# Kernel tuning notes

Hardware: AMD Instinct MI355X
Metric: run time of the kernel (lower is better)

## Reference

```python
import jax, jax.numpy as jnp
import numpy as np

N_NODES = 100000
N_EDGES = 1600000
D_IN, D_HID, D_OUT = 128, 128, 64


def setup_inputs() -> dict:
    key = jax.random.key(0)
    ks = jax.random.split(key, 6)
    x = jax.random.normal(ks[0], (N_NODES, D_IN), dtype=jnp.float32)
    edge_index = jax.random.randint(ks[1], (2, N_EDGES), 0, N_NODES, dtype=jnp.int64)
    s1 = 1.0 / np.sqrt(D_IN)
    s2 = 1.0 / np.sqrt(D_HID)
    return {
        "x": x,
        "edge_index": edge_index,
        "Wl1": jax.random.uniform(ks[2], (D_HID, D_IN), jnp.float32, -s1, s1),
        "bl1": jnp.zeros((D_HID,), jnp.float32),
        "Wr1": jax.random.uniform(ks[3], (D_HID, D_IN), jnp.float32, -s1, s1),
        "Wl2": jax.random.uniform(ks[4], (D_OUT, D_HID), jnp.float32, -s2, s2),
        "bl2": jnp.zeros((D_OUT,), jnp.float32),
        "Wr2": jax.random.uniform(ks[5], (D_OUT, D_HID), jnp.float32, -s2, s2),
    }


def _sage_conv(x, src, dst, Wl, bl, Wr, n_nodes):
    # mean-aggregate neighbor features src -> dst
    agg = jax.ops.segment_sum(x[src], dst, num_segments=n_nodes)  # [N, d_in]
    deg = jax.ops.segment_sum(jnp.ones((src.shape[0],), x.dtype), dst, num_segments=n_nodes)
    agg = agg / jnp.maximum(deg, 1.0)[:, None]
    # PyG SAGEConv: lin_l(agg) + lin_r(x), bias only on lin_l
    return agg @ Wl.T + bl + x @ Wr.T


def reference(x, edge_index, Wl1, bl1, Wr1, Wl2, bl2, Wr2):
    src, dst = edge_index[0], edge_index[1]
    n = x.shape[0]
    h = _sage_conv(x, src, dst, Wl1, bl1, Wr1, n)
    h = jax.nn.relu(h)
    # dropout is identity in eval mode (training=False)
    out = _sage_conv(h, src, dst, Wl2, bl2, Wr2, n)
    return out
```

## Files before the change

### kernel.cpp

```cpp
#include <hip/hip_runtime.h>

#define N_NODES_C 100000
#define N_EDGES_C 1600000
#define NT32_C 3125
#define NBUCK_C 392
#define BCAP_C 4800
#define EPB_C 4096

typedef __attribute__((ext_vector_type(8))) short short8;
typedef __attribute__((ext_vector_type(4))) short short4v;
typedef __attribute__((ext_vector_type(4))) float floatx4;

static __device__ __forceinline__ unsigned short f2bf(float f) {
    union { float f; unsigned int u; } c; c.f = f;
    unsigned int u = c.u;
    unsigned int lsb = (u >> 16) & 1u;
    u += 0x7fffu + lsb;
    return (unsigned short)(u >> 16);
}
static __device__ __forceinline__ float bf2f(unsigned short h) {
    union { unsigned int u; float f; } c; c.u = ((unsigned int)h) << 16;
    return c.f;
}

__global__ void bucket_kernel(const int* __restrict__ src, const int* __restrict__ dst,
                              int* __restrict__ gcur, int* __restrict__ bucket, int E) {
    __shared__ int ssrc[EPB_C];
    __shared__ int sdst[EPB_C];
    __shared__ int lcnt[NBUCK_C];
    __shared__ int lbase[NBUCK_C];
    __shared__ int lcur[NBUCK_C];
    const int tid = threadIdx.x;
    const int e0 = blockIdx.x * EPB_C;
    const int n = min(EPB_C, E - e0);

    for (int i = tid; i < NBUCK_C; i += 256) { lcnt[i] = 0; lcur[i] = 0; }
    for (int i = tid; i < n; i += 256) {
        ssrc[i] = src[e0 + i];
        sdst[i] = dst[e0 + i];
    }
    __syncthreads();
    for (int i = tid; i < n; i += 256) {
        atomicAdd(&lcnt[sdst[i] >> 8], 1);
    }
    __syncthreads();
    for (int i = tid; i < NBUCK_C; i += 256) {
        int c = lcnt[i];
        lbase[i] = (c > 0) ? atomicAdd(&gcur[i], c) : 0;
    }
    __syncthreads();
    for (int i = tid; i < n; i += 256) {
        int d = sdst[i];
        int b = d >> 8;
        int p = lbase[b] + atomicAdd(&lcur[b], 1);
        if (p < BCAP_C) bucket[b * BCAP_C + p] = (ssrc[i] << 8) | (d & 255);
    }
}

__global__ void csr_build_kernel(const int* __restrict__ gcur, const int* __restrict__ bucket,
                                 int2* __restrict__ nodeinfo, int* __restrict__ csr, int N) {
    __shared__ int sg[NBUCK_C];
    __shared__ int lcnt[256];
    __shared__ int lcur[256];
    __shared__ int sc[2][256];
    __shared__ int eord[BCAP_C];
    __shared__ int sbase_s;
    const int b = blockIdx.x;
    const int tid = threadIdx.x;
    const int ne = min(gcur[b], BCAP_C);

    for (int i = tid; i < NBUCK_C; i += 256) sg[i] = min(gcur[i], BCAP_C);
    lcnt[tid] = 0;
    lcur[tid] = 0;
    __syncthreads();
    if (tid == 0) {
        int s = 0;
        for (int i = 0; i < b; i++) s += sg[i];
        sbase_s = s;
    }
    const int* be = bucket + b * BCAP_C;
    for (int i = tid; i < ne; i += 256) {
        atomicAdd(&lcnt[be[i] & 255], 1);
    }
    __syncthreads();
    sc[0][tid] = lcnt[tid];
    __syncthreads();
    int cur = 0;
    for (int off = 1; off < 256; off <<= 1) {
        int v = sc[cur][tid] + ((tid >= off) ? sc[cur][tid - off] : 0);
        sc[1 - cur][tid] = v;
        __syncthreads();
        cur ^= 1;
    }
    for (int i = tid; i < ne; i += 256) {
        int p = be[i];
        int dl = p & 255;
        int slot = atomicAdd(&lcur[dl], 1);
        int pre = (dl == 0) ? 0 : sc[cur][dl - 1];
        eord[pre + slot] = p >> 8;
    }
    __syncthreads();
    const int sbase = sbase_s;
    for (int i = tid; i < ne; i += 256) csr[sbase + i] = eord[i];
    int node = (b << 8) + tid;
    if (node < N) {
        int pre = (tid == 0) ? 0 : sc[cur][tid - 1];
        nodeinfo[node] = make_int2(sbase + pre, lcnt[tid]);
    }
}

__global__ void prep_kernel(const float* __restrict__ Wl1, const float* __restrict__ Wr1,
                            const float* __restrict__ Wl2, const float* __restrict__ Wr2,
                            const float* __restrict__ x,
                            unsigned short* __restrict__ B1hi, unsigned short* __restrict__ B1lo,
                            unsigned short* __restrict__ B2hi, unsigned short* __restrict__ B2lo,
                            unsigned short* __restrict__ xb) {
    int blk = blockIdx.x;
    int tid = threadIdx.x;
    if (blk < 128) {
        int t = blk * 256 + tid;
        int j  = t & 7;
        int l  = (t >> 3) & 63;
        int ks = (t >> 9) & 7;
        int ct = t >> 12;
        int k = ks * 32 + ((l >> 4) << 3) + j;
        int o = ct * 16 + (l & 15);
        float v = (k < 128) ? Wl1[o * 128 + k] : Wr1[o * 128 + (k - 128)];
        unsigned short hi = f2bf(v);
        B1hi[t] = hi;
        B1lo[t] = f2bf(v - bf2f(hi));
    } else if (blk < 192) {
        int t = (blk - 128) * 256 + tid;
        int j  = t & 7;
        int l  = (t >> 3) & 63;
        int ks = (t >> 9) & 3;
        int ct = t >> 11;
        int k = ks * 32 + ((l >> 4) << 3) + j;
        int o = ct * 16 + (l & 15);
        float v = (o < 64) ? Wl2[o * 128 + k] : Wr2[(o - 64) * 128 + k];
        unsigned short hi = f2bf(v);
        B2hi[t] = hi;
        B2lo[t] = f2bf(v - bf2f(hi));
    } else {
        int t = (blk - 192) * 256 + tid;
        if (t >= N_NODES_C * 16) return;
        const float4* p = (const float4*)x;
        float4 a = p[(size_t)t * 2];
        float4 bb = p[(size_t)t * 2 + 1];
        unsigned short r[8] = {f2bf(a.x), f2bf(a.y), f2bf(a.z), f2bf(a.w),
                               f2bf(bb.x), f2bf(bb.y), f2bf(bb.z), f2bf(bb.w)};
        *(uint4*)(xb + (size_t)t * 8) = *(uint4*)r;
    }
}

static __device__ __forceinline__ void acc_add8(float* a, uint4 v) {
    unsigned int u[4] = {v.x, v.y, v.z, v.w};
#pragma unroll
    for (int i = 0; i < 4; i++) {
        union { unsigned int x; float f; } lo, hi;
        lo.x = u[i] << 16;
        hi.x = u[i] & 0xffff0000u;
        a[2 * i]     += lo.f;
        a[2 * i + 1] += hi.f;
    }
}

__global__ void agg_bf_kernel(const unsigned short* __restrict__ featb,
                              const int2* __restrict__ nodeinfo,
                              const int* __restrict__ csr,
                              unsigned short* __restrict__ aggb, int N) {
    int wid = (blockIdx.x * 256 + threadIdx.x) >> 6;
    if (wid >= N) return;
    int lane = threadIdx.x & 63;
    int q = lane >> 4;
    int c = lane & 15;
    int2 info = nodeinfo[wid];
    const int* row = csr + info.x;
    const int deg = info.y;
    float a0[8] = {0,0,0,0,0,0,0,0};
    float a1[8] = {0,0,0,0,0,0,0,0};
    float a2[8] = {0,0,0,0,0,0,0,0};
    float a3[8] = {0,0,0,0,0,0,0,0};
    int e = q;
    for (; e + 12 < deg; e += 16) {
        int s0 = row[e];
        int s1 = row[e + 4];
        int s2 = row[e + 8];
        int s3 = row[e + 12];
        uint4 v0 = *(const uint4*)(featb + (size_t)s0 * 128 + c * 8);
        uint4 v1 = *(const uint4*)(featb + (size_t)s1 * 128 + c * 8);
        uint4 v2 = *(const uint4*)(featb + (size_t)s2 * 128 + c * 8);
        uint4 v3 = *(const uint4*)(featb + (size_t)s3 * 128 + c * 8);
        acc_add8(a0, v0);
        acc_add8(a1, v1);
        acc_add8(a2, v2);
        acc_add8(a3, v3);
    }
    for (; e < deg; e += 4) {
        int s0 = row[e];
        uint4 v0 = *(const uint4*)(featb + (size_t)s0 * 128 + c * 8);
        acc_add8(a0, v0);
    }
    float acc[8];
#pragma unroll
    for (int j = 0; j < 8; j++) {
        float v = (a0[j] + a1[j]) + (a2[j] + a3[j]);
        v += __shfl_xor(v, 16, 64);
        v += __shfl_xor(v, 32, 64);
        acc[j] = v;
    }
    if (lane < 16) {
        float sc = 1.0f / fmaxf((float)deg, 1.0f);
        unsigned short r[8];
#pragma unroll
        for (int j = 0; j < 8; j++) r[j] = f2bf(acc[j] * sc);
        *(uint4*)(aggb + (size_t)wid * 128 + c * 8) = *(uint4*)r;
    }
}

__launch_bounds__(256, 2)
__global__ void gemm1_kernel(const unsigned short* __restrict__ aggb,
                             const float* __restrict__ xf,
                             const unsigned short* __restrict__ Bhi,
                             const unsigned short* __restrict__ Blo,
                             const float* __restrict__ bias,
                             unsigned short* __restrict__ hbf) {
    __shared__ unsigned short sAhi[32][264];
    __shared__ unsigned short sAlo[32][136];

    const int wave = threadIdx.x >> 6;
    const int lane = threadIdx.x & 63;
    const int quad = lane >> 4;
    const int l16 = lane & 15;

    short8 bhi[2][8], blo[2][8];
    float bias_v[2];
#pragma unroll
    for (int i = 0; i < 2; i++) {
        int ct = wave * 2 + i;
        bias_v[i] = bias[ct * 16 + l16];
#pragma unroll
        for (int ks = 0; ks < 8; ks++) {
            int off = ((ct * 8 + ks) * 64 + lane) * 8;
            bhi[i][ks] = *(const short8*)(Bhi + off);
            blo[i][ks] = *(const short8*)(Blo + off);
        }
    }

    const int tid = threadIdx.x;

    for (int tile = blockIdx.x; tile < NT32_C; tile += gridDim.x) {
        const int node0 = tile * 32;
        for (int u = tid; u < 512; u += 256) {
            int n = u >> 4, cc = u & 15;
            *(short8*)&sAhi[n][cc * 8] =
                *(const short8*)(aggb + (size_t)(node0 + n) * 128 + cc * 8);
        }
        for (int u = tid; u < 1024; u += 256) {
            int n = u >> 5, c2 = u & 31;
            float4 v = *(const float4*)(xf + (size_t)(node0 + n) * 128 + c2 * 4);
            short4v hi, lo;
            unsigned short h0 = f2bf(v.x); hi.x = (short)h0; lo.x = (short)f2bf(v.x - bf2f(h0));
            unsigned short h1 = f2bf(v.y); hi.y = (short)h1; lo.y = (short)f2bf(v.y - bf2f(h1));
            unsigned short h2 = f2bf(v.z); hi.z = (short)h2; lo.z = (short)f2bf(v.z - bf2f(h2));
            unsigned short h3 = f2bf(v.w); hi.w = (short)h3; lo.w = (short)f2bf(v.w - bf2f(h3));
            *(short4v*)&sAhi[n][128 + c2 * 4] = hi;
            *(short4v*)&sAlo[n][c2 * 4]       = lo;
        }
        __syncthreads();

        floatx4 acc[2][2];
#pragma unroll
        for (int i = 0; i < 2; i++)
#pragma unroll
            for (int s = 0; s < 2; s++)
                acc[i][s] = (floatx4){0.f, 0.f, 0.f, 0.f};

#pragma unroll
        for (int ks = 0; ks < 8; ks++) {
            short8 a0 = *(const short8*)&sAhi[l16][ks * 32 + quad * 8];
            short8 a1 = *(const short8*)&sAhi[16 + l16][ks * 32 + quad * 8];
            if (ks < 4) {
#pragma unroll
                for (int i = 0; i < 2; i++) {
                    acc[i][0] = __builtin_amdgcn_mfma_f32_16x16x32_bf16(a0, bhi[i][ks], acc[i][0], 0, 0, 0);
                    acc[i][0] = __builtin_amdgcn_mfma_f32_16x16x32_bf16(a0, blo[i][ks], acc[i][0], 0, 0, 0);
                    acc[i][1] = __builtin_amdgcn_mfma_f32_16x16x32_bf16(a1, bhi[i][ks], acc[i][1], 0, 0, 0);
                    acc[i][1] = __builtin_amdgcn_mfma_f32_16x16x32_bf16(a1, blo[i][ks], acc[i][1], 0, 0, 0);
                }
            } else {
                short8 a0l = *(const short8*)&sAlo[l16][(ks - 4) * 32 + quad * 8];
                short8 a1l = *(const short8*)&sAlo[16 + l16][(ks - 4) * 32 + quad * 8];
#pragma unroll
                for (int i = 0; i < 2; i++) {
                    acc[i][0] = __builtin_amdgcn_mfma_f32_16x16x32_bf16(a0, bhi[i][ks], acc[i][0], 0, 0, 0);
                    acc[i][0] = __builtin_amdgcn_mfma_f32_16x16x32_bf16(a0l, bhi[i][ks], acc[i][0], 0, 0, 0);
                    acc[i][0] = __builtin_amdgcn_mfma_f32_16x16x32_bf16(a0, blo[i][ks], acc[i][0], 0, 0, 0);
                    acc[i][1] = __builtin_amdgcn_mfma_f32_16x16x32_bf16(a1, bhi[i][ks], acc[i][1], 0, 0, 0);
                    acc[i][1] = __builtin_amdgcn_mfma_f32_16x16x32_bf16(a1l, bhi[i][ks], acc[i][1], 0, 0, 0);
                    acc[i][1] = __builtin_amdgcn_mfma_f32_16x16x32_bf16(a1, blo[i][ks], acc[i][1], 0, 0, 0);
                }
            }
        }

#pragma unroll
        for (int i = 0; i < 2; i++) {
            int o = wave * 32 + i * 16 + l16;
#pragma unroll
            for (int s = 0; s < 2; s++) {
                float vals[4] = {acc[i][s].x, acc[i][s].y, acc[i][s].z, acc[i][s].w};
#pragma unroll
                for (int r = 0; r < 4; r++) {
                    int node = node0 + s * 16 + quad * 4 + r;
                    float v = fmaxf(vals[r] + bias_v[i], 0.f);
                    hbf[(size_t)node * 128 + o] = f2bf(v);
                }
            }
        }
        __syncthreads();
    }
}

__launch_bounds__(256, 2)
__global__ void gemm2_kernel(const unsigned short* __restrict__ hbf,
                             const unsigned short* __restrict__ Bhi,
                             const unsigned short* __restrict__ Blo,
                             const float* __restrict__ bias,
                             unsigned short* __restrict__ g,
                             unsigned short* __restrict__ s2b) {
    __shared__ unsigned short sA[32][136];

    const int wave = threadIdx.x >> 6;
    const int lane = threadIdx.x & 63;
    const int quad = lane >> 4;
    const int l16 = lane & 15;

    short8 bhi[2][4], blo[2][4];
    float bias_v[2];
#pragma unroll
    for (int i = 0; i < 2; i++) {
        int ct = wave * 2 + i;
        int o = ct * 16 + l16;
        bias_v[i] = (o >= 64) ? bias[o - 64] : 0.f;
#pragma unroll
        for (int ks = 0; ks < 4; ks++) {
            int off = ((ct * 4 + ks) * 64 + lane) * 8;
            bhi[i][ks] = *(const short8*)(Bhi + off);
            blo[i][ks] = *(const short8*)(Blo + off);
        }
    }

    const int tid = threadIdx.x;

    for (int tile = blockIdx.x; tile < NT32_C; tile += gridDim.x) {
        const int node0 = tile * 32;
        for (int u = tid; u < 512; u += 256) {
            int n = u >> 4, cc = u & 15;
            *(short8*)&sA[n][cc * 8] =
                *(const short8*)(hbf + (size_t)(node0 + n) * 128 + cc * 8);
        }
        __syncthreads();

        floatx4 acc[2][2];
#pragma unroll
        for (int i = 0; i < 2; i++)
#pragma unroll
            for (int s = 0; s < 2; s++)
                acc[i][s] = (floatx4){0.f, 0.f, 0.f, 0.f};

#pragma unroll
        for (int ks = 0; ks < 4; ks++) {
            short8 a0 = *(const short8*)&sA[l16][ks * 32 + quad * 8];
            short8 a1 = *(const short8*)&sA[16 + l16][ks * 32 + quad * 8];
#pragma unroll
            for (int i = 0; i < 2; i++) {
                acc[i][0] = __builtin_amdgcn_mfma_f32_16x16x32_bf16(a0, bhi[i][ks], acc[i][0], 0, 0, 0);
                acc[i][0] = __builtin_amdgcn_mfma_f32_16x16x32_bf16(a0, blo[i][ks], acc[i][0], 0, 0, 0);
                acc[i][1] = __builtin_amdgcn_mfma_f32_16x16x32_bf16(a1, bhi[i][ks], acc[i][1], 0, 0, 0);
                acc[i][1] = __builtin_amdgcn_mfma_f32_16x16x32_bf16(a1, blo[i][ks], acc[i][1], 0, 0, 0);
            }
        }

#pragma unroll
        for (int i = 0; i < 2; i++) {
            int o = wave * 32 + i * 16 + l16;
#pragma unroll
            for (int s = 0; s < 2; s++) {
                float vals[4] = {acc[i][s].x, acc[i][s].y, acc[i][s].z, acc[i][s].w};
#pragma unroll
                for (int r = 0; r < 4; r++) {
                    int node = node0 + s * 16 + quad * 4 + r;
                    float v = vals[r] + bias_v[i];
                    if (o < 64) g[(size_t)node * 64 + o] = f2bf(v);
                    else        s2b[(size_t)node * 64 + (o - 64)] = f2bf(v);
                }
            }
        }
        __syncthreads();
    }
}

static __device__ __forceinline__ void acc_add4(float* a, uint2 v) {
    unsigned int u[2] = {v.x, v.y};
#pragma unroll
    for (int i = 0; i < 2; i++) {
        union { unsigned int x; float f; } lo, hi;
        lo.x = u[i] << 16;
        hi.x = u[i] & 0xffff0000u;
        a[2 * i]     += lo.f;
        a[2 * i + 1] += hi.f;
    }
}

__global__ void agg2e_kernel(const unsigned short* __restrict__ g,
                             const unsigned short* __restrict__ s2b,
                             const int2* __restrict__ nodeinfo,
                             const int* __restrict__ csr,
                             float* __restrict__ out, int N) {
    int wid = (blockIdx.x * 256 + threadIdx.x) >> 6;
    if (wid >= N) return;
    int lane = threadIdx.x & 63;
    int q = lane >> 4;
    int c = lane & 15;
    int2 info = nodeinfo[wid];
    const int* row = csr + info.x;
    const int deg = info.y;
    float a0[4] = {0,0,0,0};
    float a1[4] = {0,0,0,0};
    float a2[4] = {0,0,0,0};
    float a3[4] = {0,0,0,0};
    int e = q;
    for (; e + 12 < deg; e += 16) {
        int s0 = row[e];
        int s1 = row[e + 4];
        int s2 = row[e + 8];
        int s3 = row[e + 12];
        uint2 v0 = *(const uint2*)(g + (size_t)s0 * 64 + c * 4);
        uint2 v1 = *(const uint2*)(g + (size_t)s1 * 64 + c * 4);
        uint2 v2 = *(const uint2*)(g + (size_t)s2 * 64 + c * 4);
        uint2 v3 = *(const uint2*)(g + (size_t)s3 * 64 + c * 4);
        acc_add4(a0, v0);
        acc_add4(a1, v1);
        acc_add4(a2, v2);
        acc_add4(a3, v3);
    }
    for (; e < deg; e += 4) {
        int s0 = row[e];
        uint2 v0 = *(const uint2*)(g + (size_t)s0 * 64 + c * 4);
        acc_add4(a0, v0);
    }
    float acc[4];
#pragma unroll
    for (int j = 0; j < 4; j++) {
        float v = (a0[j] + a1[j]) + (a2[j] + a3[j]);
        v += __shfl_xor(v, 16, 64);
        v += __shfl_xor(v, 32, 64);
        acc[j] = v;
    }
    if (lane < 16) {
        float sc = 1.0f / fmaxf((float)deg, 1.0f);
        uint2 sv = *(const uint2*)(s2b + (size_t)wid * 64 + c * 4);
        float s[4];
        {
            union { unsigned int x; float f; } t0, t1, t2, t3;
            t0.x = sv.x << 16; t1.x = sv.x & 0xffff0000u;
            t2.x = sv.y << 16; t3.x = sv.y & 0xffff0000u;
            s[0] = t0.f; s[1] = t1.f; s[2] = t2.f; s[3] = t3.f;
        }
        float4 r;
        r.x = acc[0] * sc + s[0];
        r.y = acc[1] * sc + s[1];
        r.z = acc[2] * sc + s[2];
        r.w = acc[3] * sc + s[3];
        *(float4*)(out + (size_t)wid * 64 + c * 4) = r;
    }
}

extern "C" void kernel_launch(void* const* d_in, const int* in_sizes, int n_in,
                              void* d_out, int out_size, void* d_ws, size_t ws_size,
                              hipStream_t stream) {
    const float* x    = (const float*)d_in[0];
    const int*   ei   = (const int*)d_in[1];
    const float* Wl1  = (const float*)d_in[2];
    const float* bl1  = (const float*)d_in[3];
    const float* Wr1  = (const float*)d_in[4];
    const float* Wl2  = (const float*)d_in[5];
    const float* bl2  = (const float*)d_in[6];
    const float* Wr2  = (const float*)d_in[7];
    float* out = (float*)d_out;

    const int N = N_NODES_C;
    const int E = N_EDGES_C;
    const int* src = ei;
    const int* dst = ei + E;

    char* ws = (char*)d_ws;
    unsigned short* B1hi = (unsigned short*)(ws + 0);
    unsigned short* B1lo = (unsigned short*)(ws + 65536);
    unsigned short* B2hi = (unsigned short*)(ws + 131072);
    unsigned short* B2lo = (unsigned short*)(ws + 163840);
    int2*  nodeinfo = (int2*)(ws + 196608);
    int*   gcur = (int*)  (ws + 998400);
    int*   csr  = (int*)  (ws + 1048576);
    unsigned short* xbf  = (unsigned short*)(ws + 20248576);
    unsigned short* aggb = (unsigned short*)(ws + 45848576);
    unsigned short* hbf  = (unsigned short*)(ws + 71448576);
    unsigned short* g    = aggb;
    unsigned short* s2b  = aggb + 6400000;
    int*   bucket = (int*)hbf;

    hipMemsetAsync(gcur, 0, NBUCK_C * sizeof(int), stream);
    bucket_kernel<<<(E + EPB_C - 1) / EPB_C, 256, 0, stream>>>(src, dst, gcur, bucket, E);
    csr_build_kernel<<<NBUCK_C, 256, 0, stream>>>(gcur, bucket, nodeinfo, csr, N);

    prep_kernel<<<192 + (N * 16 + 255) / 256, 256, 0, stream>>>(
        Wl1, Wr1, Wl2, Wr2, x, B1hi, B1lo, B2hi, B2lo, xbf);

    agg_bf_kernel<<<(N + 3) / 4, 256, 0, stream>>>(xbf, nodeinfo, csr, aggb, N);
    gemm1_kernel<<<512, 256, 0, stream>>>(aggb, x, B1hi, B1lo, bl1, hbf);

    gemm2_kernel<<<512, 256, 0, stream>>>(hbf, B2hi, B2lo, bl2, g, s2b);
    agg2e_kernel<<<(N + 3) / 4, 256, 0, stream>>>(g, s2b, nodeinfo, csr, out, N);
}
```

Measured before the change: 299.6 us.

## Switch pipeline from split-bf16 to single fp16 storage and MFMA

Replaces the hi/lo bf16 split weights and activations with single fp16 values, so both GEMMs issue one f16 MFMA per tile instead of two or three bf16 MFMAs. gemm1 now reads the precomputed fp16 x instead of converting fp32 x inline. The aggregation kernels accumulate with fdot2 and use two accumulators instead of four. The bucket kernel halves edges per block and drops its shared staging. fp16 narrows the exponent range compared with bf16 and drops the extra precision the split provided, so accuracy margins shrink.

```diff
diff --git a/kernel.cpp b/kernel.cpp
--- a/kernel.cpp
+++ b/kernel.cpp
@@ -5,28 +5,21 @@
 #define NT32_C 3125
 #define NBUCK_C 392
 #define BCAP_C 4800
-#define EPB_C 4096
-
-typedef __attribute__((ext_vector_type(8))) short short8;
-typedef __attribute__((ext_vector_type(4))) short short4v;
+#define EPB_C 2048
+
+typedef _Float16 half_t;
+typedef __attribute__((ext_vector_type(2))) _Float16 half2v;
+typedef __attribute__((ext_vector_type(8))) _Float16 half8v;
 typedef __attribute__((ext_vector_type(4))) float floatx4;
 
-static __device__ __forceinline__ unsigned short f2bf(float f) {
-    union { float f; unsigned int u; } c; c.f = f;
-    unsigned int u = c.u;
-    unsigned int lsb = (u >> 16) & 1u;
-    u += 0x7fffu + lsb;
-    return (unsigned short)(u >> 16);
-}
-static __device__ __forceinline__ float bf2f(unsigned short h) {
-    union { unsigned int u; float f; } c; c.u = ((unsigned int)h) << 16;
-    return c.f;
-}
+#if defined(__has_builtin)
+#if __has_builtin(__builtin_amdgcn_fdot2)
+#define HAS_FDOT2 1
+#endif
+#endif
 
 __global__ void bucket_kernel(const int* __restrict__ src, const int* __restrict__ dst,
                               int* __restrict__ gcur, int* __restrict__ bucket, int E) {
-    __shared__ int ssrc[EPB_C];
-    __shared__ int sdst[EPB_C];
     __shared__ int lcnt[NBUCK_C];
     __shared__ int lbase[NBUCK_C];
     __shared__ int lcur[NBUCK_C];
@@ -35,13 +28,9 @@
     const int n = min(EPB_C, E - e0);
 
     for (int i = tid; i < NBUCK_C; i += 256) { lcnt[i] = 0; lcur[i] = 0; }
+    __syncthreads();
     for (int i = tid; i < n; i += 256) {
-        ssrc[i] = src[e0 + i];
-        sdst[i] = dst[e0 + i];
-    }
-    __syncthreads();
-    for (int i = tid; i < n; i += 256) {
-        atomicAdd(&lcnt[sdst[i] >> 8], 1);
+        atomicAdd(&lcnt[dst[e0 + i] >> 8], 1);
     }
     __syncthreads();
     for (int i = tid; i < NBUCK_C; i += 256) {
@@ -50,10 +39,11 @@
     }
     __syncthreads();
     for (int i = tid; i < n; i += 256) {
-        int d = sdst[i];
+        int d = dst[e0 + i];
+        int s = src[e0 + i];
         int b = d >> 8;
         int p = lbase[b] + atomicAdd(&lcur[b], 1);
-        if (p < BCAP_C) bucket[b * BCAP_C + p] = (ssrc[i] << 8) | (d & 255);
+        if (p < BCAP_C) bucket[b * BCAP_C + p] = (s << 8) | (d & 255);
     }
 }
 
@@ -112,9 +102,8 @@
 __global__ void prep_kernel(const float* __restrict__ Wl1, const float* __restrict__ Wr1,
                             const float* __restrict__ Wl2, const float* __restrict__ Wr2,
                             const float* __restrict__ x,
-                            unsigned short* __restrict__ B1hi, unsigned short* __restrict__ B1lo,
-                            unsigned short* __restrict__ B2hi, unsigned short* __restrict__ B2lo,
-                            unsigned short* __restrict__ xb) {
+                            half_t* __restrict__ B1, half_t* __restrict__ B2,
+                            half_t* __restrict__ xh) {
     int blk = blockIdx.x;
     int tid = threadIdx.x;
     if (blk < 128) {
@@ -126,9 +115,7 @@
         int k = ks * 32 + ((l >> 4) << 3) + j;
         int o = ct * 16 + (l & 15);
         float v = (k < 128) ? Wl1[o * 128 + k] : Wr1[o * 128 + (k - 128)];
-        unsigned short hi = f2bf(v);
-        B1hi[t] = hi;
-        B1lo[t] = f2bf(v - bf2f(hi));
+        B1[t] = (half_t)v;
     } else if (blk < 192) {
         int t = (blk - 128) * 256 + tid;
         int j  = t & 7;
@@ -138,37 +125,65 @@
         int k = ks * 32 + ((l >> 4) << 3) + j;
         int o = ct * 16 + (l & 15);
         float v = (o < 64) ? Wl2[o * 128 + k] : Wr2[(o - 64) * 128 + k];
-        unsigned short hi = f2bf(v);
-        B2hi[t] = hi;
-        B2lo[t] = f2bf(v - bf2f(hi));
+        B2[t] = (half_t)v;
     } else {
         int t = (blk - 192) * 256 + tid;
         if (t >= N_NODES_C * 16) return;
         const float4* p = (const float4*)x;
         float4 a = p[(size_t)t * 2];
-        float4 bb = p[(size_t)t * 2 + 1];
-        unsigned short r[8] = {f2bf(a.x), f2bf(a.y), f2bf(a.z), f2bf(a.w),
-                               f2bf(bb.x), f2bf(bb.y), f2bf(bb.z), f2bf(bb.w)};
-        *(uint4*)(xb + (size_t)t * 8) = *(uint4*)r;
-    }
-}
-
-static __device__ __forceinline__ void acc_add8(float* a, uint4 v) {
+        float4 b = p[(size_t)t * 2 + 1];
+        half_t r[8] = {(half_t)a.x, (half_t)a.y, (half_t)a.z, (half_t)a.w,
+                       (half_t)b.x, (half_t)b.y, (half_t)b.z, (half_t)b.w};
+        *(uint4*)(xh + (size_t)t * 8) = *(uint4*)r;
+    }
+}
+
+static __device__ __forceinline__ void dot8(float* a, uint4 v) {
     unsigned int u[4] = {v.x, v.y, v.z, v.w};
+#ifdef HAS_FDOT2
+    const half2v e0 = {(half_t)1.0f, (half_t)0.0f};
+    const half2v e1 = {(half_t)0.0f, (half_t)1.0f};
 #pragma unroll
     for (int i = 0; i < 4; i++) {
-        union { unsigned int x; float f; } lo, hi;
-        lo.x = u[i] << 16;
-        hi.x = u[i] & 0xffff0000u;
-        a[2 * i]     += lo.f;
-        a[2 * i + 1] += hi.f;
-    }
-}
-
-__global__ void agg_bf_kernel(const unsigned short* __restrict__ featb,
-                              const int2* __restrict__ nodeinfo,
-                              const int* __restrict__ csr,
-                              unsigned short* __restrict__ aggb, int N) {
+        union { unsigned int x; half2v h; } c; c.x = u[i];
+        a[2 * i]     = __builtin_amdgcn_fdot2(c.h, e0, a[2 * i], false);
+        a[2 * i + 1] = __builtin_amdgcn_fdot2(c.h, e1, a[2 * i + 1], false);
+    }
+#else
+#pragma unroll
+    for (int i = 0; i < 4; i++) {
+        union { unsigned int x; half2v h; } c; c.x = u[i];
+        a[2 * i]     += (float)c.h.x;
+        a[2 * i + 1] += (float)c.h.y;
+    }
+#endif
+}
+
+static __device__ __forceinline__ void dot4(float* a, uint2 v) {
+    unsigned int u[2] = {v.x, v.y};
+#ifdef HAS_FDOT2
+    const half2v e0 = {(half_t)1.0f, (half_t)0.0f};
+    const half2v e1 = {(half_t)0.0f, (half_t)1.0f};
+#pragma unroll
+    for (int i = 0; i < 2; i++) {
+        union { unsigned int x; half2v h; } c; c.x = u[i];
+        a[2 * i]     = __builtin_amdgcn_fdot2(c.h, e0, a[2 * i], false);
+        a[2 * i + 1] = __builtin_amdgcn_fdot2(c.h, e1, a[2 * i + 1], false);
+    }
+#else
+#pragma unroll
+    for (int i = 0; i < 2; i++) {
+        union { unsigned int x; half2v h; } c; c.x = u[i];
+        a[2 * i]     += (float)c.h.x;
+        a[2 * i + 1] += (float)c.h.y;
+    }
+#endif
+}
+
+__global__ void agg1_kernel(const half_t* __restrict__ xh,
+                            const int2* __restrict__ nodeinfo,
+                            const int* __restrict__ csr,
+                            half_t* __restrict__ aggh, int N) {
     int wid = (blockIdx.x * 256 + threadIdx.x) >> 6;
     if (wid >= N) return;
     int lane = threadIdx.x & 63;
@@ -179,61 +194,51 @@
     const int deg = info.y;
     float a0[8] = {0,0,0,0,0,0,0,0};
     float a1[8] = {0,0,0,0,0,0,0,0};
-    float a2[8] = {0,0,0,0,0,0,0,0};
-    float a3[8] = {0,0,0,0,0,0,0,0};
     int e = q;
-    for (; e + 12 < deg; e += 16) {
+    for (; e + 4 < deg; e += 8) {
         int s0 = row[e];
         int s1 = row[e + 4];
-        int s2 = row[e + 8];
-        int s3 = row[e + 12];
-        uint4 v0 = *(const uint4*)(featb + (size_t)s0 * 128 + c * 8);
-        uint4 v1 = *(const uint4*)(featb + (size_t)s1 * 128 + c * 8);
-        uint4 v2 = *(const uint4*)(featb + (size_t)s2 * 128 + c * 8);
-        uint4 v3 = *(const uint4*)(featb + (size_t)s3 * 128 + c * 8);
-        acc_add8(a0, v0);
-        acc_add8(a1, v1);
-        acc_add8(a2, v2);
-        acc_add8(a3, v3);
-    }
-    for (; e < deg; e += 4) {
+        uint4 v0 = *(const uint4*)(xh + (size_t)s0 * 128 + c * 8);
+        uint4 v1 = *(const uint4*)(xh + (size_t)s1 * 128 + c * 8);
+        dot8(a0, v0);
+        dot8(a1, v1);
+    }
+    if (e < deg) {
         int s0 = row[e];
-        uint4 v0 = *(const uint4*)(featb + (size_t)s0 * 128 + c * 8);
-        acc_add8(a0, v0);
+        uint4 v0 = *(const uint4*)(xh + (size_t)s0 * 128 + c * 8);
+        dot8(a0, v0);
     }
     float acc[8];
 #pragma unroll
     for (int j = 0; j < 8; j++) {
-        float v = (a0[j] + a1[j]) + (a2[j] + a3[j]);
+        float v = a0[j] + a1[j];
         v += __shfl_xor(v, 16, 64);
         v += __shfl_xor(v, 32, 64);
         acc[j] = v;
     }
     if (lane < 16) {
         float sc = 1.0f / fmaxf((float)deg, 1.0f);
-        unsigned short r[8];
-#pragma unroll
-        for (int j = 0; j < 8; j++) r[j] = f2bf(acc[j] * sc);
-        *(uint4*)(aggb + (size_t)wid * 128 + c * 8) = *(uint4*)r;
+        half_t r[8];
+#pragma unroll
+        for (int j = 0; j < 8; j++) r[j] = (half_t)(acc[j] * sc);
+        *(uint4*)(aggh + (size_t)wid * 128 + c * 8) = *(uint4*)r;
     }
 }
 
 __launch_bounds__(256, 2)
-__global__ void gemm1_kernel(const unsigned short* __restrict__ aggb,
-                             const float* __restrict__ xf,
-                             const unsigned short* __restrict__ Bhi,
-                             const unsigned short* __restrict__ Blo,
+__global__ void gemm1_kernel(const half_t* __restrict__ aggh,
+                             const half_t* __restrict__ xh,
+                             const half_t* __restrict__ B1,
                              const float* __restrict__ bias,
-                             unsigned short* __restrict__ hbf) {
-    __shared__ unsigned short sAhi[32][264];
-    __shared__ unsigned short sAlo[32][136];
+                             half_t* __restrict__ hh) {
+    __shared__ half_t sA[32][264];
 
     const int wave = threadIdx.x >> 6;
     const int lane = threadIdx.x & 63;
     const int quad = lane >> 4;
     const int l16 = lane & 15;
 
-    short8 bhi[2][8], blo[2][8];
+    half8v bf[2][8];
     float bias_v[2];
 #pragma unroll
     for (int i = 0; i < 2; i++) {
@@ -241,9 +246,7 @@
         bias_v[i] = bias[ct * 16 + l16];
 #pragma unroll
         for (int ks = 0; ks < 8; ks++) {
-            int off = ((ct * 8 + ks) * 64 + lane) * 8;
-            bhi[i][ks] = *(const short8*)(Bhi + off);
-            blo[i][ks] = *(const short8*)(Blo + off);
+            bf[i][ks] = *(const half8v*)(B1 + ((ct * 8 + ks) * 64 + lane) * 8);
         }
     }
 
@@ -253,19 +256,10 @@
         const int node0 = tile * 32;
         for (int u = tid; u < 512; u += 256) {
             int n = u >> 4, cc = u & 15;
-            *(short8*)&sAhi[n][cc * 8] =
-                *(const short8*)(aggb + (size_t)(node0 + n) * 128 + cc * 8);
-        }
-        for (int u = tid; u < 1024; u += 256) {
-            int n = u >> 5, c2 = u & 31;
-            float4 v = *(const float4*)(xf + (size_t)(node0 + n) * 128 + c2 * 4);
-            short4v hi, lo;
-            unsigned short h0 = f2bf(v.x); hi.x = (short)h0; lo.x = (short)f2bf(v.x - bf2f(h0));
-            unsigned short h1 = f2bf(v.y); hi.y = (short)h1; lo.y = (short)f2bf(v.y - bf2f(h1));
-            unsigned short h2 = f2bf(v.z); hi.z = (short)h2; lo.z = (short)f2bf(v.z - bf2f(h2));
-            unsigned short h3 = f2bf(v.w); hi.w = (short)h3; lo.w = (short)f2bf(v.w - bf2f(h3));
-            *(short4v*)&sAhi[n][128 + c2 * 4] = hi;
-            *(short4v*)&sAlo[n][c2 * 4]       = lo;
+            *(half8v*)&sA[n][cc * 8] =
+                *(const half8v*)(aggh + (size_t)(node0 + n) * 128 + cc * 8);
+            *(half8v*)&sA[n][128 + cc * 8] =
+                *(const half8v*)(xh + (size_t)(node0 + n) * 128 + cc * 8);
         }
         __syncthreads();
 
@@ -278,28 +272,12 @@
 
 #pragma unroll
         for (int ks = 0; ks < 8; ks++) {
-            short8 a0 = *(const short8*)&sAhi[l16][ks * 32 + quad * 8];
-            short8 a1 = *(const short8*)&sAhi[16 + l16][ks * 32 + quad * 8];
-            if (ks < 4) {
-#pragma unroll
-                for (int i = 0; i < 2; i++) {
-                    acc[i][0] = __builtin_amdgcn_mfma_f32_16x16x32_bf16(a0, bhi[i][ks], acc[i][0], 0, 0, 0);
-                    acc[i][0] = __builtin_amdgcn_mfma_f32_16x16x32_bf16(a0, blo[i][ks], acc[i][0], 0, 0, 0);
-                    acc[i][1] = __builtin_amdgcn_mfma_f32_16x16x32_bf16(a1, bhi[i][ks], acc[i][1], 0, 0, 0);
-                    acc[i][1] = __builtin_amdgcn_mfma_f32_16x16x32_bf16(a1, blo[i][ks], acc[i][1], 0, 0, 0);
-                }
-            } else {
-                short8 a0l = *(const short8*)&sAlo[l16][(ks - 4) * 32 + quad * 8];
-                short8 a1l = *(const short8*)&sAlo[16 + l16][(ks - 4) * 32 + quad * 8];
-#pragma unroll
-                for (int i = 0; i < 2; i++) {
-                    acc[i][0] = __builtin_amdgcn_mfma_f32_16x16x32_bf16(a0, bhi[i][ks], acc[i][0], 0, 0, 0);
-                    acc[i][0] = __builtin_amdgcn_mfma_f32_16x16x32_bf16(a0l, bhi[i][ks], acc[i][0], 0, 0, 0);
-                    acc[i][0] = __builtin_amdgcn_mfma_f32_16x16x32_bf16(a0, blo[i][ks], acc[i][0], 0, 0, 0);
-                    acc[i][1] = __builtin_amdgcn_mfma_f32_16x16x32_bf16(a1, bhi[i][ks], acc[i][1], 0, 0, 0);
-                    acc[i][1] = __builtin_amdgcn_mfma_f32_16x16x32_bf16(a1l, bhi[i][ks], acc[i][1], 0, 0, 0);
-                    acc[i][1] = __builtin_amdgcn_mfma_f32_16x16x32_bf16(a1, blo[i][ks], acc[i][1], 0, 0, 0);
-                }
+            half8v a0 = *(const half8v*)&sA[l16][ks * 32 + quad * 8];
+            half8v a1 = *(const half8v*)&sA[16 + l16][ks * 32 + quad * 8];
+#pragma unroll
+            for (int i = 0; i < 2; i++) {
+                acc[i][0] = __builtin_amdgcn_mfma_f32_16x16x32_f16(a0, bf[i][ks], acc[i][0], 0, 0, 0);
+                acc[i][1] = __builtin_amdgcn_mfma_f32_16x16x32_f16(a1, bf[i][ks], acc[i][1], 0, 0, 0);
             }
         }
 
@@ -313,7 +291,7 @@
                 for (int r = 0; r < 4; r++) {
                     int node = node0 + s * 16 + quad * 4 + r;
                     float v = fmaxf(vals[r] + bias_v[i], 0.f);
-                    hbf[(size_t)node * 128 + o] = f2bf(v);
+                    hh[(size_t)node * 128 + o] = (half_t)v;
                 }
             }
         }
@@ -322,20 +300,19 @@
 }
 
 __launch_bounds__(256, 2)
-__global__ void gemm2_kernel(const unsigned short* __restrict__ hbf,
-                             const unsigned short* __restrict__ Bhi,
-                             const unsigned short* __restrict__ Blo,
+__global__ void gemm2_kernel(const half_t* __restrict__ hh,
+                             const half_t* __restrict__ B2,
                              const float* __restrict__ bias,
-                             unsigned short* __restrict__ g,
-                             unsigned short* __restrict__ s2b) {
-    __shared__ unsigned short sA[32][136];
+                             half_t* __restrict__ g,
+                             half_t* __restrict__ s2h) {
+    __shared__ half_t sA[32][136];
 
     const int wave = threadIdx.x >> 6;
     const int lane = threadIdx.x & 63;
     const int quad = lane >> 4;
     const int l16 = lane & 15;
 
-    short8 bhi[2][4], blo[2][4];
+    half8v bf[2][4];
     float bias_v[2];
 #pragma unroll
     for (int i = 0; i < 2; i++) {
@@ -344,9 +321,7 @@
         bias_v[i] = (o >= 64) ? bias[o - 64] : 0.f;
 #pragma unroll
         for (int ks = 0; ks < 4; ks++) {
-            int off = ((ct * 4 + ks) * 64 + lane) * 8;
-            bhi[i][ks] = *(const short8*)(Bhi + off);
-            blo[i][ks] = *(const short8*)(Blo + off);
+            bf[i][ks] = *(const half8v*)(B2 + ((ct * 4 + ks) * 64 + lane) * 8);
         }
     }
 
@@ -356,8 +331,8 @@
         const int node0 = tile * 32;
         for (int u = tid; u < 512; u += 256) {
             int n = u >> 4, cc = u & 15;
-            *(short8*)&sA[n][cc * 8] =
-                *(const short8*)(hbf + (size_t)(node0 + n) * 128 + cc * 8);
+            *(half8v*)&sA[n][cc * 8] =
+                *(const half8v*)(hh + (size_t)(node0 + n) * 128 + cc * 8);
         }
         __syncthreads();
 
@@ -370,14 +345,12 @@
 
 #pragma unroll
         for (int ks = 0; ks < 4; ks++) {
-            short8 a0 = *(const short8*)&sA[l16][ks * 32 + quad * 8];
-            short8 a1 = *(const short8*)&sA[16 + l16][ks * 32 + quad * 8];
+            half8v a0 = *(const half8v*)&sA[l16][ks * 32 + quad * 8];
+            half8v a1 = *(const half8v*)&sA[16 + l16][ks * 32 + quad * 8];
 #pragma unroll
             for (int i = 0; i < 2; i++) {
-                acc[i][0] = __builtin_amdgcn_mfma_f32_16x16x32_bf16(a0, bhi[i][ks], acc[i][0], 0, 0, 0);
-                acc[i][0] = __builtin_amdgcn_mfma_f32_16x16x32_bf16(a0, blo[i][ks], acc[i][0], 0, 0, 0);
-                acc[i][1] = __builtin_amdgcn_mfma_f32_16x16x32_bf16(a1, bhi[i][ks], acc[i][1], 0, 0, 0);
-                acc[i][1] = __builtin_amdgcn_mfma_f32_16x16x32_bf16(a1, blo[i][ks], acc[i][1], 0, 0, 0);
+                acc[i][0] = __builtin_amdgcn_mfma_f32_16x16x32_f16(a0, bf[i][ks], acc[i][0], 0, 0, 0);
+                acc[i][1] = __builtin_amdgcn_mfma_f32_16x16x32_f16(a1, bf[i][ks], acc[i][1], 0, 0, 0);
             }
         }
 
@@ -391,8 +364,8 @@
                 for (int r = 0; r < 4; r++) {
                     int node = node0 + s * 16 + quad * 4 + r;
                     float v = vals[r] + bias_v[i];
-                    if (o < 64) g[(size_t)node * 64 + o] = f2bf(v);
-                    else        s2b[(size_t)node * 64 + (o - 64)] = f2bf(v);
+                    if (o < 64) g[(size_t)node * 64 + o] = (half_t)v;
+                    else        s2h[(size_t)node * 64 + (o - 64)] = (half_t)v;
                 }
             }
         }
@@ -400,20 +373,8 @@
     }
 }
 
-static __device__ __forceinline__ void acc_add4(float* a, uint2 v) {
-    unsigned int u[2] = {v.x, v.y};
-#pragma unroll
-    for (int i = 0; i < 2; i++) {
-        union { unsigned int x; float f; } lo, hi;
-        lo.x = u[i] << 16;
-        hi.x = u[i] & 0xffff0000u;
-        a[2 * i]     += lo.f;
-        a[2 * i + 1] += hi.f;
-    }
-}
-
-__global__ void agg2e_kernel(const unsigned short* __restrict__ g,
-                             const unsigned short* __restrict__ s2b,
+__global__ void agg2e_kernel(const half_t* __restrict__ g,
+                             const half_t* __restrict__ s2h,
                              const int2* __restrict__ nodeinfo,
                              const int* __restrict__ csr,
                              float* __restrict__ out, int N) {
@@ -427,51 +388,38 @@
     const int deg = info.y;
     float a0[4] = {0,0,0,0};
     float a1[4] = {0,0,0,0};
-    float a2[4] = {0,0,0,0};
-    float a3[4] = {0,0,0,0};
     int e = q;
-    for (; e + 12 < deg; e += 16) {
+    for (; e + 4 < deg; e += 8) {
         int s0 = row[e];
         int s1 = row[e + 4];
-        int s2 = row[e + 8];
-        int s3 = row[e + 12];
         uint2 v0 = *(const uint2*)(g + (size_t)s0 * 64 + c * 4);
         uint2 v1 = *(const uint2*)(g + (size_t)s1 * 64 + c * 4);
-        uint2 v2 = *(const uint2*)(g + (size_t)s2 * 64 + c * 4);
-        uint2 v3 = *(const uint2*)(g + (size_t)s3 * 64 + c * 4);
-        acc_add4(a0, v0);
-        acc_add4(a1, v1);
-        acc_add4(a2, v2);
-        acc_add4(a3, v3);
-    }
-    for (; e < deg; e += 4) {
+        dot4(a0, v0);
+        dot4(a1, v1);
+    }
+    if (e < deg) {
         int s0 = row[e];
         uint2 v0 = *(const uint2*)(g + (size_t)s0 * 64 + c * 4);
-        acc_add4(a0, v0);
+        dot4(a0, v0);
     }
     float acc[4];
 #pragma unroll
     for (int j = 0; j < 4; j++) {
-        float v = (a0[j] + a1[j]) + (a2[j] + a3[j]);
+        float v = a0[j] + a1[j];
         v += __shfl_xor(v, 16, 64);
         v += __shfl_xor(v, 32, 64);
         acc[j] = v;
     }
     if (lane < 16) {
         float sc = 1.0f / fmaxf((float)deg, 1.0f);
-        uint2 sv = *(const uint2*)(s2b + (size_t)wid * 64 + c * 4);
-        float s[4];
-        {
-            union { unsigned int x; float f; } t0, t1, t2, t3;
-            t0.x = sv.x << 16; t1.x = sv.x & 0xffff0000u;
-            t2.x = sv.y << 16; t3.x = sv.y & 0xffff0000u;
-            s[0] = t0.f; s[1] = t1.f; s[2] = t2.f; s[3] = t3.f;
-        }
+        uint2 sv = *(const uint2*)(s2h + (size_t)wid * 64 + c * 4);
+        union { unsigned int x; half2v h; } c0, c1;
+        c0.x = sv.x; c1.x = sv.y;
         float4 r;
-        r.x = acc[0] * sc + s[0];
-        r.y = acc[1] * sc + s[1];
-        r.z = acc[2] * sc + s[2];
-        r.w = acc[3] * sc + s[3];
+        r.x = acc[0] * sc + (float)c0.h.x;
+        r.y = acc[1] * sc + (float)c0.h.y;
+        r.z = acc[2] * sc + (float)c1.h.x;
+        r.w = acc[3] * sc + (float)c1.h.y;
         *(float4*)(out + (size_t)wid * 64 + c * 4) = r;
     }
 }
@@ -495,30 +443,28 @@
     const int* dst = ei + E;
 
     char* ws = (char*)d_ws;
-    unsigned short* B1hi = (unsigned short*)(ws + 0);
-    unsigned short* B1lo = (unsigned short*)(ws + 65536);
-    unsigned short* B2hi = (unsigned short*)(ws + 131072);
-    unsigned short* B2lo = (unsigned short*)(ws + 163840);
-    int2*  nodeinfo = (int2*)(ws + 196608);
-    int*   gcur = (int*)  (ws + 998400);
-    int*   csr  = (int*)  (ws + 1048576);
-    unsigned short* xbf  = (unsigned short*)(ws + 20248576);
-    unsigned short* aggb = (unsigned short*)(ws + 45848576);
-    unsigned short* hbf  = (unsigned short*)(ws + 71448576);
-    unsigned short* g    = aggb;
-    unsigned short* s2b  = aggb + 6400000;
-    int*   bucket = (int*)hbf;
+    half_t* B1   = (half_t*)(ws + 0);
+    half_t* B2   = (half_t*)(ws + 65536);
+    int*    gcur = (int*)   (ws + 98304);
+    int2*   nodeinfo = (int2*)(ws + 102400);
+    int*    csr  = (int*)   (ws + 1048576);
+    half_t* xh   = (half_t*)(ws + 7448576);
+    half_t* aggh = (half_t*)(ws + 33048576);
+    half_t* hh   = (half_t*)(ws + 58648576);
+    half_t* g    = aggh;
+    half_t* s2h  = aggh + 6400000;
+    int*    bucket = (int*)hh;
 
     hipMemsetAsync(gcur, 0, NBUCK_C * sizeof(int), stream);
     bucket_kernel<<<(E + EPB_C - 1) / EPB_C, 256, 0, stream>>>(src, dst, gcur, bucket, E);
     csr_build_kernel<<<NBUCK_C, 256, 0, stream>>>(gcur, bucket, nodeinfo, csr, N);
 
     prep_kernel<<<192 + (N * 16 + 255) / 256, 256, 0, stream>>>(
-        Wl1, Wr1, Wl2, Wr2, x, B1hi, B1lo, B2hi, B2lo, xbf);
-
-    agg_bf_kernel<<<(N + 3) / 4, 256, 0, stream>>>(xbf, nodeinfo, csr, aggb, N);
-    gemm1_kernel<<<512, 256, 0, stream>>>(aggb, x, B1hi, B1lo, bl1, hbf);
-
-    gemm2_kernel<<<512, 256, 0, stream>>>(hbf, B2hi, B2lo, bl2, g, s2b);
-    agg2e_kernel<<<(N + 3) / 4, 256, 0, stream>>>(g, s2b, nodeinfo, csr, out, N);
-}
+        Wl1, Wr1, Wl2, Wr2, x, B1, B2, xh);
+
+    agg1_kernel<<<(N + 3) / 4, 256, 0, stream>>>(xh, nodeinfo, csr, aggh, N);
+    gemm1_kernel<<<512, 256, 0, stream>>>(aggh, xh, B1, bl1, hh);
+
+    gemm2_kernel<<<512, 256, 0, stream>>>(hh, B2, bl2, g, s2h);
+    agg2e_kernel<<<(N + 3) / 4, 256, 0, stream>>>(g, s2h, nodeinfo, csr, out, N);
+}
```

After: 289.7 us. 3.3% less time.
